# Kernel tuning notes

Measured on AMD Instinct MI355X. Metric: run time of the kernel, lower is better.

## Reference

```python
import jax, jax.numpy as jnp
import numpy as np

B, D, A, M = 262144, 128, 32, 100


def setup_inputs() -> dict:
    key = jax.random.key(0)
    ks = jax.random.split(key, 8)
    s = 0.05
    return {
        "state": jax.random.normal(ks[0], (B, D), jnp.float32),
        "action": jax.random.normal(ks[1], (B, A), jnp.float32),
        "next_state": jax.random.normal(ks[2], (B, D), jnp.float32),
        "seen": jax.random.normal(ks[3], (M, D), jnp.float32),
        "W1": jax.random.normal(ks[4], (D, D + A), jnp.float32) * s,
        "b1": jnp.zeros((D,), jnp.float32),
        "W2": jax.random.normal(ks[5], (D, D), jnp.float32) * s,
        "b2": jnp.zeros((D,), jnp.float32),
        "Wf": jax.random.normal(ks[6], (D, D), jnp.float32) * s,
        "bf": jnp.zeros((D,), jnp.float32),
    }


def reference(state, action, next_state, seen, W1, b1, W2, b2, Wf, bf):
    # predictor: Linear(D+A -> D) -> ReLU -> Linear(D -> D)   (torch: y = x W^T + b)
    x = jnp.concatenate([state, action], axis=-1)            # [B, D+A]
    h = jax.nn.relu(x @ W1.T + b1)                           # [B, D]
    predicted_next = h @ W2.T + b2                           # [B, D]

    # feature_extractor: Linear(D -> D) -> ReLU
    feat = lambda z: jax.nn.relu(z @ Wf.T + bf)
    features_actual = feat(next_state)                       # [B, D]
    features_pred = feat(predicted_next)                     # [B, D]

    # per-sample MSE prediction error (features_actual detached in original)
    fa_sg = jax.lax.stop_gradient(features_actual)
    pred_error = jnp.mean((features_pred - fa_sg) ** 2, axis=-1)  # [B]

    # 1-NN L2 distance to memory buffer, batched via the ||a-b||^2 expansion
    # (avoids materializing [B, M, D])
    a2 = jnp.sum(features_actual ** 2, axis=-1, keepdims=True)    # [B, 1]
    s2 = jnp.sum(seen ** 2, axis=-1)                              # [M]
    d2 = a2 + s2[None, :] - 2.0 * (features_actual @ seen.T)      # [B, M]
    min_dist = jnp.sqrt(jnp.maximum(jnp.min(d2, axis=-1), 0.0))   # [B]
    novelty = jnp.minimum(1.0, min_dist / 10.0)                   # [B]

    curiosity_reward = pred_error * 0.5 + novelty * 0.5
    return jnp.stack([pred_error, novelty, curiosity_reward])     # [3, B]
```

## Files before the change

### kernel.cpp

```cpp
#include <hip/hip_runtime.h>
#include <hip/hip_bf16.h>
#include <math.h>

#define B_TOT 262144

typedef __attribute__((ext_vector_type(8))) short v8s;
typedef __attribute__((ext_vector_type(4))) float v4f;

#define WS_W1 0
#define WS_W2 20480
#define WS_WF 36864
#define WS_SEEN 53248
#define WS_S2_BYTES 135168

__device__ __forceinline__ unsigned short f2bf(float f) {
  union { float f; unsigned u; } cv; cv.f = f;
  unsigned u = cv.u;
  return (unsigned short)((u + 0x7FFFu + ((u >> 16) & 1u)) >> 16);
}
__device__ __forceinline__ float bf2f(unsigned short h) {
  union { unsigned u; float f; } cv; cv.u = ((unsigned)h) << 16;
  return cv.f;
}
__device__ __forceinline__ unsigned f2bf2(float x, float y) {
  float2 f; f.x = x; f.y = y;
  __hip_bfloat162 h = __float22bfloat162_rn(f);
  union { __hip_bfloat162 h; unsigned u; } cv; cv.h = h;
  return cv.u;
}

__global__ void curiosity_prep(const float* __restrict__ W1, const float* __restrict__ W2,
                               const float* __restrict__ Wf, const float* __restrict__ seen,
                               unsigned short* __restrict__ wsb, float* __restrict__ s2) {
  int bid = blockIdx.x;
  if (bid < 264) {
    int idx = bid * 256 + (int)threadIdx.x;
    if (idx < 20480) {
      int f = idx >> 9, r = idx & 511, L = r >> 3, j = r & 7;
      int t = f / 5, c = f - t * 5;
      int n = t * 16 + (L & 15), k = c * 32 + (L >> 4) * 8 + j;
      wsb[idx] = f2bf(W1[n * 160 + k]);
    } else if (idx < 36864) {
      int e = idx - 20480;
      int f = e >> 9, r = e & 511, L = r >> 3, j = r & 7;
      int t = f >> 2, c = f & 3;
      int n = t * 16 + (L & 15), k = c * 32 + (L >> 4) * 8 + j;
      wsb[idx] = f2bf(W2[n * 128 + k]);
    } else if (idx < 53248) {
      int e = idx - 36864;
      int f = e >> 9, r = e & 511, L = r >> 3, j = r & 7;
      int t = f >> 2, c = f & 3;
      int n = t * 16 + (L & 15), k = c * 32 + (L >> 4) * 8 + j;
      wsb[idx] = f2bf(Wf[n * 128 + k]);
    } else {
      int e = idx - 53248;
      int f = e >> 9, r = e & 511, L = r >> 3, j = r & 7;
      int t = f >> 2, c = f & 3;
      int n = t * 16 + (L & 15), k = c * 32 + (L >> 4) * 8 + j;
      float v = (n < 100) ? seen[n * 128 + k] : 0.f;
      wsb[idx] = f2bf(v);
    }
  } else {
    int wv = (int)threadIdx.x >> 6, lane = (int)threadIdx.x & 63;
    int mm = (bid - 264) * 4 + wv;
    float s;
    if (mm < 100) {
      float v0 = seen[mm * 128 + lane], v1 = seen[mm * 128 + 64 + lane];
      s = v0 * v0 + v1 * v1;
#pragma unroll
      for (int msk = 1; msk < 64; msk <<= 1) s += __shfl_xor(s, msk, 64);
    } else {
      s = 1e30f;
    }
    if (lane == 0) s2[mm] = s;
  }
}

__device__ __forceinline__ void stage16x128(const float* __restrict__ src,
                                            unsigned short* buf, int lane) {
  float4 v[8];
#pragma unroll
  for (int i = 0; i < 8; ++i) {
    int flat = i * 64 + lane;
    v[i] = *(const float4*)(src + (flat >> 5) * 128 + (flat & 31) * 4);
  }
#pragma unroll
  for (int i = 0; i < 8; ++i) {
    int flat = i * 64 + lane;
    uint2 p;
    p.x = f2bf2(v[i].x, v[i].y);
    p.y = f2bf2(v[i].z, v[i].w);
    *(uint2*)(buf + (flat >> 5) * 136 + (flat & 31) * 4) = p;
  }
}
__device__ __forceinline__ void stage16x32(const float* __restrict__ src,
                                           unsigned short* buf, int lane) {
  float4 v[2];
#pragma unroll
  for (int i = 0; i < 2; ++i) {
    int flat = i * 64 + lane;
    v[i] = *(const float4*)(src + (flat >> 3) * 32 + (flat & 7) * 4);
  }
#pragma unroll
  for (int i = 0; i < 2; ++i) {
    int flat = i * 64 + lane;
    uint2 p;
    p.x = f2bf2(v[i].x, v[i].y);
    p.y = f2bf2(v[i].z, v[i].w);
    *(uint2*)(buf + (flat >> 3) * 136 + (flat & 7) * 4) = p;
  }
}
__device__ __forceinline__ v8s read_frag(const unsigned short* buf, int m, int q, int c) {
  return *(const v8s*)(buf + m * 136 + c * 32 + q * 8);
}
__device__ __forceinline__ v8s wfrag(const unsigned short* __restrict__ wsb,
                                     int base, int fragIdx, int lane) {
  return *(const v8s*)(wsb + base + fragIdx * 512 + lane * 8);
}

__global__ __launch_bounds__(256, 3) void curiosity_main(
    const float* __restrict__ state, const float* __restrict__ action,
    const float* __restrict__ next_state,
    const float* __restrict__ b1, const float* __restrict__ b2,
    const float* __restrict__ bfv,
    const unsigned short* __restrict__ wsb, const float* __restrict__ s2g,
    float* __restrict__ out) {
  __shared__ __attribute__((aligned(16))) unsigned short s_int[4][2][2176];
  __shared__ float s_o[3][128];

  const int tid = (int)threadIdx.x;
  const int w = tid >> 6, lane = tid & 63;
  const int m = lane & 15, q = lane >> 4;
  const int rowblk = (int)blockIdx.x * 128 + w * 32;

  unsigned short* buf[2] = { &s_int[w][0][0], &s_int[w][1][0] };

  float bv1[8];
#pragma unroll
  for (int tg = 0; tg < 8; ++tg) bv1[tg] = b1[tg * 16 + m];

  v8s a1[2][5];
  stage16x32(action + (size_t)(rowblk) * 32, buf[0], lane);
  stage16x32(action + (size_t)(rowblk + 16) * 32, buf[1], lane);
  a1[0][4] = *(const v8s*)(buf[0] + m * 136 + q * 8);
  a1[1][4] = *(const v8s*)(buf[1] + m * 136 + q * 8);
  stage16x128(state + (size_t)(rowblk) * 128, buf[0], lane);
  stage16x128(state + (size_t)(rowblk + 16) * 128, buf[1], lane);
#pragma unroll
  for (int c = 0; c < 4; ++c) {
    a1[0][c] = read_frag(buf[0], m, q, c);
    a1[1][c] = read_frag(buf[1], m, q, c);
  }

  float bv2[8];
#pragma unroll
  for (int tg = 0; tg < 8; ++tg) bv2[tg] = b2[tg * 16 + m];

#pragma unroll
  for (int hf = 0; hf < 2; ++hf) {
    v8s bfr[20];
#pragma unroll
    for (int c = 0; c < 5; ++c)
#pragma unroll
      for (int tl = 0; tl < 4; ++tl)
        bfr[c * 4 + tl] = wfrag(wsb, WS_W1, (hf * 4 + tl) * 5 + c, lane);
    v4f acc[2][4] = {};
#pragma unroll
    for (int c = 0; c < 5; ++c)
#pragma unroll
      for (int tl = 0; tl < 4; ++tl) {
        acc[0][tl] = __builtin_amdgcn_mfma_f32_16x16x32_bf16(a1[0][c], bfr[c * 4 + tl], acc[0][tl], 0, 0, 0);
        acc[1][tl] = __builtin_amdgcn_mfma_f32_16x16x32_bf16(a1[1][c], bfr[c * 4 + tl], acc[1][tl], 0, 0, 0);
      }
#pragma unroll
    for (int tl = 0; tl < 4; ++tl) {
      int tg = hf * 4 + tl;
      float bv = bv1[tg];
#pragma unroll
      for (int tt = 0; tt < 2; ++tt)
#pragma unroll
        for (int r = 0; r < 4; r += 2) {
          unsigned p = f2bf2(fmaxf(acc[tt][tl][r] + bv, 0.f),
                             fmaxf(acc[tt][tl][r + 1] + bv, 0.f));
          buf[tt][(q * 4 + r) * 136 + tg * 16 + m] = (unsigned short)p;
          buf[tt][(q * 4 + r + 1) * 136 + tg * 16 + m] = (unsigned short)(p >> 16);
        }
    }
  }

  v8s af[2][4];
#pragma unroll
  for (int c = 0; c < 4; ++c) {
    af[0][c] = read_frag(buf[0], m, q, c);
    af[1][c] = read_frag(buf[1], m, q, c);
  }
  float bvf[8];
#pragma unroll
  for (int tg = 0; tg < 8; ++tg) bvf[tg] = bfv[tg * 16 + m];

#pragma unroll
  for (int hf = 0; hf < 2; ++hf) {
    v8s bfr[16];
#pragma unroll
    for (int c = 0; c < 4; ++c)
#pragma unroll
      for (int tl = 0; tl < 4; ++tl)
        bfr[c * 4 + tl] = wfrag(wsb, WS_W2, (hf * 4 + tl) * 4 + c, lane);
    v4f acc[2][4] = {};
#pragma unroll
    for (int c = 0; c < 4; ++c)
#pragma unroll
      for (int tl = 0; tl < 4; ++tl) {
        acc[0][tl] = __builtin_amdgcn_mfma_f32_16x16x32_bf16(af[0][c], bfr[c * 4 + tl], acc[0][tl], 0, 0, 0);
        acc[1][tl] = __builtin_amdgcn_mfma_f32_16x16x32_bf16(af[1][c], bfr[c * 4 + tl], acc[1][tl], 0, 0, 0);
      }
#pragma unroll
    for (int tl = 0; tl < 4; ++tl) {
      int tg = hf * 4 + tl;
      float bv = bv2[tg];
#pragma unroll
      for (int tt = 0; tt < 2; ++tt)
#pragma unroll
        for (int r = 0; r < 4; r += 2) {
          unsigned p = f2bf2(acc[tt][tl][r] + bv, acc[tt][tl][r + 1] + bv);
          buf[tt][(q * 4 + r) * 136 + tg * 16 + m] = (unsigned short)p;
          buf[tt][(q * 4 + r + 1) * 136 + tg * 16 + m] = (unsigned short)(p >> 16);
        }
    }
  }

  v8s a4[2][4], a3[2][4];
#pragma unroll
  for (int c = 0; c < 4; ++c) {
    a4[0][c] = read_frag(buf[0], m, q, c);
    a4[1][c] = read_frag(buf[1], m, q, c);
  }
  stage16x128(next_state + (size_t)(rowblk) * 128, buf[0], lane);
  stage16x128(next_state + (size_t)(rowblk + 16) * 128, buf[1], lane);
#pragma unroll
  for (int c = 0; c < 4; ++c) {
    a3[0][c] = read_frag(buf[0], m, q, c);
    a3[1][c] = read_frag(buf[1], m, q, c);
  }

  float s2v[7];
#pragma unroll
  for (int tl = 0; tl < 7; ++tl) s2v[tl] = s2g[tl * 16 + m];

  unsigned fa_pk[2][16];
  float a2s[2][4] = {};
#pragma unroll
  for (int hf = 0; hf < 2; ++hf) {
    v8s bfr[16];
#pragma unroll
    for (int c = 0; c < 4; ++c)
#pragma unroll
      for (int tl = 0; tl < 4; ++tl)
        bfr[c * 4 + tl] = wfrag(wsb, WS_WF, (hf * 4 + tl) * 4 + c, lane);
    v4f acc[2][4] = {};
#pragma unroll
    for (int c = 0; c < 4; ++c)
#pragma unroll
      for (int tl = 0; tl < 4; ++tl) {
        acc[0][tl] = __builtin_amdgcn_mfma_f32_16x16x32_bf16(a3[0][c], bfr[c * 4 + tl], acc[0][tl], 0, 0, 0);
        acc[1][tl] = __builtin_amdgcn_mfma_f32_16x16x32_bf16(a3[1][c], bfr[c * 4 + tl], acc[1][tl], 0, 0, 0);
      }
#pragma unroll
    for (int tl = 0; tl < 4; ++tl) {
      int tg = hf * 4 + tl;
      float bv = bvf[tg];
#pragma unroll
      for (int tt = 0; tt < 2; ++tt)
#pragma unroll
        for (int rp = 0; rp < 2; ++rp) {
          int r = rp * 2;
          unsigned p = f2bf2(fmaxf(acc[tt][tl][r] + bv, 0.f),
                             fmaxf(acc[tt][tl][r + 1] + bv, 0.f));
          fa_pk[hf][tl * 4 + tt * 2 + rp] = p;
          buf[tt][(q * 4 + r) * 136 + tg * 16 + m] = (unsigned short)p;
          buf[tt][(q * 4 + r + 1) * 136 + tg * 16 + m] = (unsigned short)(p >> 16);
          float flo = bf2f((unsigned short)p), fhi = bf2f((unsigned short)(p >> 16));
          a2s[tt][r] += flo * flo;
          a2s[tt][r + 1] += fhi * fhi;
        }
    }
  }

  float pe[2][4] = {};
#pragma unroll
  for (int hf = 0; hf < 2; ++hf) {
    v8s bfr[16];
#pragma unroll
    for (int c = 0; c < 4; ++c)
#pragma unroll
      for (int tl = 0; tl < 4; ++tl)
        bfr[c * 4 + tl] = wfrag(wsb, WS_WF, (hf * 4 + tl) * 4 + c, lane);
    v4f acc[2][4] = {};
#pragma unroll
    for (int c = 0; c < 4; ++c)
#pragma unroll
      for (int tl = 0; tl < 4; ++tl) {
        acc[0][tl] = __builtin_amdgcn_mfma_f32_16x16x32_bf16(a4[0][c], bfr[c * 4 + tl], acc[0][tl], 0, 0, 0);
        acc[1][tl] = __builtin_amdgcn_mfma_f32_16x16x32_bf16(a4[1][c], bfr[c * 4 + tl], acc[1][tl], 0, 0, 0);
      }
#pragma unroll
    for (int tl = 0; tl < 4; ++tl) {
      int tg = hf * 4 + tl;
      float bv = bvf[tg];
#pragma unroll
      for (int tt = 0; tt < 2; ++tt)
#pragma unroll
        for (int rp = 0; rp < 2; ++rp) {
          int r = rp * 2;
          unsigned p = fa_pk[hf][tl * 4 + tt * 2 + rp];
          float d0 = fmaxf(acc[tt][tl][r] + bv, 0.f) - bf2f((unsigned short)p);
          float d1 = fmaxf(acc[tt][tl][r + 1] + bv, 0.f) - bf2f((unsigned short)(p >> 16));
          pe[tt][r] += d0 * d0;
          pe[tt][r + 1] += d1 * d1;
        }
    }
  }

#pragma unroll
  for (int tt = 0; tt < 2; ++tt)
#pragma unroll
    for (int r = 0; r < 4; ++r)
#pragma unroll
      for (int msk = 1; msk < 16; msk <<= 1) {
        pe[tt][r] += __shfl_xor(pe[tt][r], msk, 16);
        a2s[tt][r] += __shfl_xor(a2s[tt][r], msk, 16);
      }

  v8s a5[2][4];
#pragma unroll
  for (int c = 0; c < 4; ++c) {
    a5[0][c] = read_frag(buf[0], m, q, c);
    a5[1][c] = read_frag(buf[1], m, q, c);
  }
  float dmin[2][4] = {{3.4e38f, 3.4e38f, 3.4e38f, 3.4e38f},
                      {3.4e38f, 3.4e38f, 3.4e38f, 3.4e38f}};
  {
    v8s bfr[16];
#pragma unroll
    for (int tl = 0; tl < 4; ++tl)
#pragma unroll
      for (int c = 0; c < 4; ++c)
        bfr[tl * 4 + c] = wfrag(wsb, WS_SEEN, tl * 4 + c, lane);
#pragma unroll
    for (int tl = 0; tl < 4; ++tl) {
      v4f g0 = {}, g1 = {};
#pragma unroll
      for (int c = 0; c < 4; ++c) {
        g0 = __builtin_amdgcn_mfma_f32_16x16x32_bf16(a5[0][c], bfr[tl * 4 + c], g0, 0, 0, 0);
        g1 = __builtin_amdgcn_mfma_f32_16x16x32_bf16(a5[1][c], bfr[tl * 4 + c], g1, 0, 0, 0);
      }
      float s2x = s2v[tl];
#pragma unroll
      for (int r = 0; r < 4; ++r) {
        dmin[0][r] = fminf(dmin[0][r], a2s[0][r] + s2x - 2.f * g0[r]);
        dmin[1][r] = fminf(dmin[1][r], a2s[1][r] + s2x - 2.f * g1[r]);
      }
    }
  }
  {
    v8s bfr[12];
#pragma unroll
    for (int tl = 0; tl < 3; ++tl)
#pragma unroll
      for (int c = 0; c < 4; ++c)
        bfr[tl * 4 + c] = wfrag(wsb, WS_SEEN, (tl + 4) * 4 + c, lane);
#pragma unroll
    for (int tl = 0; tl < 3; ++tl) {
      v4f g0 = {}, g1 = {};
#pragma unroll
      for (int c = 0; c < 4; ++c) {
        g0 = __builtin_amdgcn_mfma_f32_16x16x32_bf16(a5[0][c], bfr[tl * 4 + c], g0, 0, 0, 0);
        g1 = __builtin_amdgcn_mfma_f32_16x16x32_bf16(a5[1][c], bfr[tl * 4 + c], g1, 0, 0, 0);
      }
      float s2x = s2v[tl + 4];
#pragma unroll
      for (int r = 0; r < 4; ++r) {
        dmin[0][r] = fminf(dmin[0][r], a2s[0][r] + s2x - 2.f * g0[r]);
        dmin[1][r] = fminf(dmin[1][r], a2s[1][r] + s2x - 2.f * g1[r]);
      }
    }
  }
#pragma unroll
  for (int tt = 0; tt < 2; ++tt)
#pragma unroll
    for (int r = 0; r < 4; ++r)
#pragma unroll
      for (int msk = 1; msk < 16; msk <<= 1)
        dmin[tt][r] = fminf(dmin[tt][r], __shfl_xor(dmin[tt][r], msk, 16));

  if (m == 0) {
#pragma unroll
    for (int tt = 0; tt < 2; ++tt)
#pragma unroll
      for (int r = 0; r < 4; ++r) {
        int rl = w * 32 + tt * 16 + q * 4 + r;
        float p = pe[tt][r] * (1.f / 128.f);
        float nov = fminf(1.f, sqrtf(fmaxf(dmin[tt][r], 0.f)) * 0.1f);
        s_o[0][rl] = p;
        s_o[1][rl] = nov;
        s_o[2][rl] = 0.5f * (p + nov);
      }
  }
  __syncthreads();
  const size_t base = (size_t)blockIdx.x * 128;
  for (int idx = tid; idx < 384; idx += 256) {
    int j = idx >> 7, r = idx & 127;
    out[(size_t)j * B_TOT + base + r] = s_o[j][r];
  }
}

extern "C" void kernel_launch(void* const* d_in, const int* in_sizes, int n_in,
                              void* d_out, int out_size, void* d_ws, size_t ws_size,
                              hipStream_t stream) {
  const float* state      = (const float*)d_in[0];
  const float* action     = (const float*)d_in[1];
  const float* next_state = (const float*)d_in[2];
  const float* seen       = (const float*)d_in[3];
  const float* W1         = (const float*)d_in[4];
  const float* b1         = (const float*)d_in[5];
  const float* W2         = (const float*)d_in[6];
  const float* b2         = (const float*)d_in[7];
  const float* Wf         = (const float*)d_in[8];
  const float* bf_        = (const float*)d_in[9];

  unsigned short* wsb = (unsigned short*)d_ws;
  float* s2 = (float*)((char*)d_ws + WS_S2_BYTES);

  curiosity_prep<<<292, 256, 0, stream>>>(W1, W2, Wf, seen, wsb, s2);
  curiosity_main<<<2048, 256, 0, stream>>>(state, action, next_state, b1, b2, bf_,
                                           wsb, s2, (float*)d_out);
}
```

Before: 375.7 us.

## Load inputs directly into MFMA fragments, prefetch next_state, fuse feature GEMMs

Result: no change. 371.8 us (-1.0%).

```diff
diff --git a/kernel.cpp b/kernel.cpp
--- a/kernel.cpp
+++ b/kernel.cpp
@@ -76,40 +76,15 @@
   }
 }
 
-__device__ __forceinline__ void stage16x128(const float* __restrict__ src,
-                                            unsigned short* buf, int lane) {
-  float4 v[8];
-#pragma unroll
-  for (int i = 0; i < 8; ++i) {
-    int flat = i * 64 + lane;
-    v[i] = *(const float4*)(src + (flat >> 5) * 128 + (flat & 31) * 4);
-  }
-#pragma unroll
-  for (int i = 0; i < 8; ++i) {
-    int flat = i * 64 + lane;
-    uint2 p;
-    p.x = f2bf2(v[i].x, v[i].y);
-    p.y = f2bf2(v[i].z, v[i].w);
-    *(uint2*)(buf + (flat >> 5) * 136 + (flat & 31) * 4) = p;
-  }
-}
-__device__ __forceinline__ void stage16x32(const float* __restrict__ src,
-                                           unsigned short* buf, int lane) {
-  float4 v[2];
-#pragma unroll
-  for (int i = 0; i < 2; ++i) {
-    int flat = i * 64 + lane;
-    v[i] = *(const float4*)(src + (flat >> 3) * 32 + (flat & 7) * 4);
-  }
-#pragma unroll
-  for (int i = 0; i < 2; ++i) {
-    int flat = i * 64 + lane;
-    uint2 p;
-    p.x = f2bf2(v[i].x, v[i].y);
-    p.y = f2bf2(v[i].z, v[i].w);
-    *(uint2*)(buf + (flat >> 3) * 136 + (flat & 7) * 4) = p;
-  }
-}
+__device__ __forceinline__ v8s cvt_frag(float4 lo, float4 hi) {
+  union { v8s v; unsigned u[4]; } r;
+  r.u[0] = f2bf2(lo.x, lo.y);
+  r.u[1] = f2bf2(lo.z, lo.w);
+  r.u[2] = f2bf2(hi.x, hi.y);
+  r.u[3] = f2bf2(hi.z, hi.w);
+  return r.v;
+}
+
 __device__ __forceinline__ v8s read_frag(const unsigned short* buf, int m, int q, int c) {
   return *(const v8s*)(buf + m * 136 + c * 32 + q * 8);
 }
@@ -135,26 +110,40 @@
 
   unsigned short* buf[2] = { &s_int[w][0][0], &s_int[w][1][0] };
 
-  float bv1[8];
+  const float* st0 = state + (size_t)(rowblk + m) * 128 + q * 8;
+  const float* st1 = st0 + 16 * 128;
+  const float* ac0 = action + (size_t)(rowblk + m) * 32 + q * 8;
+  const float* ac1 = ac0 + 16 * 32;
+  const float* np0 = next_state + (size_t)(rowblk + m) * 128 + q * 8;
+  const float* np1 = np0 + 16 * 128;
+
+  float4 sv[2][4][2], av[2][2];
+#pragma unroll
+  for (int c = 0; c < 4; ++c) {
+    sv[0][c][0] = *(const float4*)(st0 + c * 32);
+    sv[0][c][1] = *(const float4*)(st0 + c * 32 + 4);
+    sv[1][c][0] = *(const float4*)(st1 + c * 32);
+    sv[1][c][1] = *(const float4*)(st1 + c * 32 + 4);
+  }
+  av[0][0] = *(const float4*)(ac0); av[0][1] = *(const float4*)(ac0 + 4);
+  av[1][0] = *(const float4*)(ac1); av[1][1] = *(const float4*)(ac1 + 4);
+
+  float bv1[8], bv2[8], bvf[8];
 #pragma unroll
   for (int tg = 0; tg < 8; ++tg) bv1[tg] = b1[tg * 16 + m];
+#pragma unroll
+  for (int tg = 0; tg < 8; ++tg) bv2[tg] = b2[tg * 16 + m];
+#pragma unroll
+  for (int tg = 0; tg < 8; ++tg) bvf[tg] = bfv[tg * 16 + m];
 
   v8s a1[2][5];
-  stage16x32(action + (size_t)(rowblk) * 32, buf[0], lane);
-  stage16x32(action + (size_t)(rowblk + 16) * 32, buf[1], lane);
-  a1[0][4] = *(const v8s*)(buf[0] + m * 136 + q * 8);
-  a1[1][4] = *(const v8s*)(buf[1] + m * 136 + q * 8);
-  stage16x128(state + (size_t)(rowblk) * 128, buf[0], lane);
-  stage16x128(state + (size_t)(rowblk + 16) * 128, buf[1], lane);
-#pragma unroll
-  for (int c = 0; c < 4; ++c) {
-    a1[0][c] = read_frag(buf[0], m, q, c);
-    a1[1][c] = read_frag(buf[1], m, q, c);
-  }
-
-  float bv2[8];
-#pragma unroll
-  for (int tg = 0; tg < 8; ++tg) bv2[tg] = b2[tg * 16 + m];
+#pragma unroll
+  for (int c = 0; c < 4; ++c) {
+    a1[0][c] = cvt_frag(sv[0][c][0], sv[0][c][1]);
+    a1[1][c] = cvt_frag(sv[1][c][0], sv[1][c][1]);
+  }
+  a1[0][4] = cvt_frag(av[0][0], av[0][1]);
+  a1[1][4] = cvt_frag(av[1][0], av[1][1]);
 
 #pragma unroll
   for (int hf = 0; hf < 2; ++hf) {
@@ -188,18 +177,31 @@
     }
   }
 
+  float4 n0v[4][2], n1v[4][2];
+#pragma unroll
+  for (int c = 0; c < 4; ++c) {
+    n0v[c][0] = *(const float4*)(np0 + c * 32);
+    n0v[c][1] = *(const float4*)(np0 + c * 32 + 4);
+  }
+
   v8s af[2][4];
 #pragma unroll
   for (int c = 0; c < 4; ++c) {
     af[0][c] = read_frag(buf[0], m, q, c);
     af[1][c] = read_frag(buf[1], m, q, c);
   }
-  float bvf[8];
-#pragma unroll
-  for (int tg = 0; tg < 8; ++tg) bvf[tg] = bfv[tg * 16 + m];
-
+  v8s a3[2][4];
 #pragma unroll
   for (int hf = 0; hf < 2; ++hf) {
+    if (hf == 1) {
+#pragma unroll
+      for (int c = 0; c < 4; ++c) a3[0][c] = cvt_frag(n0v[c][0], n0v[c][1]);
+#pragma unroll
+      for (int c = 0; c < 4; ++c) {
+        n1v[c][0] = *(const float4*)(np1 + c * 32);
+        n1v[c][1] = *(const float4*)(np1 + c * 32 + 4);
+      }
+    }
     v8s bfr[16];
 #pragma unroll
     for (int c = 0; c < 4; ++c)
@@ -229,95 +231,59 @@
     }
   }
 
-  v8s a4[2][4], a3[2][4];
+  v8s a4[2][4];
 #pragma unroll
   for (int c = 0; c < 4; ++c) {
     a4[0][c] = read_frag(buf[0], m, q, c);
     a4[1][c] = read_frag(buf[1], m, q, c);
   }
-  stage16x128(next_state + (size_t)(rowblk) * 128, buf[0], lane);
-  stage16x128(next_state + (size_t)(rowblk + 16) * 128, buf[1], lane);
-#pragma unroll
-  for (int c = 0; c < 4; ++c) {
-    a3[0][c] = read_frag(buf[0], m, q, c);
-    a3[1][c] = read_frag(buf[1], m, q, c);
-  }
+#pragma unroll
+  for (int c = 0; c < 4; ++c) a3[1][c] = cvt_frag(n1v[c][0], n1v[c][1]);
 
   float s2v[7];
 #pragma unroll
   for (int tl = 0; tl < 7; ++tl) s2v[tl] = s2g[tl * 16 + m];
 
-  unsigned fa_pk[2][16];
+  float pe[2][4] = {};
   float a2s[2][4] = {};
 #pragma unroll
   for (int hf = 0; hf < 2; ++hf) {
-    v8s bfr[16];
-#pragma unroll
-    for (int c = 0; c < 4; ++c)
-#pragma unroll
-      for (int tl = 0; tl < 4; ++tl)
-        bfr[c * 4 + tl] = wfrag(wsb, WS_WF, (hf * 4 + tl) * 4 + c, lane);
-    v4f acc[2][4] = {};
-#pragma unroll
-    for (int c = 0; c < 4; ++c)
-#pragma unroll
-      for (int tl = 0; tl < 4; ++tl) {
-        acc[0][tl] = __builtin_amdgcn_mfma_f32_16x16x32_bf16(a3[0][c], bfr[c * 4 + tl], acc[0][tl], 0, 0, 0);
-        acc[1][tl] = __builtin_amdgcn_mfma_f32_16x16x32_bf16(a3[1][c], bfr[c * 4 + tl], acc[1][tl], 0, 0, 0);
-      }
 #pragma unroll
     for (int tl = 0; tl < 4; ++tl) {
+      v8s bfr[4];
+#pragma unroll
+      for (int c = 0; c < 4; ++c)
+        bfr[c] = wfrag(wsb, WS_WF, (hf * 4 + tl) * 4 + c, lane);
+      v4f fa0 = {}, fa1 = {}, fp0 = {}, fp1 = {};
+#pragma unroll
+      for (int c = 0; c < 4; ++c) {
+        fa0 = __builtin_amdgcn_mfma_f32_16x16x32_bf16(a3[0][c], bfr[c], fa0, 0, 0, 0);
+        fa1 = __builtin_amdgcn_mfma_f32_16x16x32_bf16(a3[1][c], bfr[c], fa1, 0, 0, 0);
+        fp0 = __builtin_amdgcn_mfma_f32_16x16x32_bf16(a4[0][c], bfr[c], fp0, 0, 0, 0);
+        fp1 = __builtin_amdgcn_mfma_f32_16x16x32_bf16(a4[1][c], bfr[c], fp1, 0, 0, 0);
+      }
       int tg = hf * 4 + tl;
       float bv = bvf[tg];
 #pragma unroll
-      for (int tt = 0; tt < 2; ++tt)
+      for (int tt = 0; tt < 2; ++tt) {
+        const v4f& fav = tt ? fa1 : fa0;
+        const v4f& fpv = tt ? fp1 : fp0;
 #pragma unroll
         for (int rp = 0; rp < 2; ++rp) {
           int r = rp * 2;
-          unsigned p = f2bf2(fmaxf(acc[tt][tl][r] + bv, 0.f),
-                             fmaxf(acc[tt][tl][r + 1] + bv, 0.f));
-          fa_pk[hf][tl * 4 + tt * 2 + rp] = p;
+          unsigned p = f2bf2(fmaxf(fav[r] + bv, 0.f),
+                             fmaxf(fav[r + 1] + bv, 0.f));
           buf[tt][(q * 4 + r) * 136 + tg * 16 + m] = (unsigned short)p;
           buf[tt][(q * 4 + r + 1) * 136 + tg * 16 + m] = (unsigned short)(p >> 16);
           float flo = bf2f((unsigned short)p), fhi = bf2f((unsigned short)(p >> 16));
           a2s[tt][r] += flo * flo;
           a2s[tt][r + 1] += fhi * fhi;
-        }
-    }
-  }
-
-  float pe[2][4] = {};
-#pragma unroll
-  for (int hf = 0; hf < 2; ++hf) {
-    v8s bfr[16];
-#pragma unroll
-    for (int c = 0; c < 4; ++c)
-#pragma unroll
-      for (int tl = 0; tl < 4; ++tl)
-        bfr[c * 4 + tl] = wfrag(wsb, WS_WF, (hf * 4 + tl) * 4 + c, lane);
-    v4f acc[2][4] = {};
-#pragma unroll
-    for (int c = 0; c < 4; ++c)
-#pragma unroll
-      for (int tl = 0; tl < 4; ++tl) {
-        acc[0][tl] = __builtin_amdgcn_mfma_f32_16x16x32_bf16(a4[0][c], bfr[c * 4 + tl], acc[0][tl], 0, 0, 0);
-        acc[1][tl] = __builtin_amdgcn_mfma_f32_16x16x32_bf16(a4[1][c], bfr[c * 4 + tl], acc[1][tl], 0, 0, 0);
-      }
-#pragma unroll
-    for (int tl = 0; tl < 4; ++tl) {
-      int tg = hf * 4 + tl;
-      float bv = bvf[tg];
-#pragma unroll
-      for (int tt = 0; tt < 2; ++tt)
-#pragma unroll
-        for (int rp = 0; rp < 2; ++rp) {
-          int r = rp * 2;
-          unsigned p = fa_pk[hf][tl * 4 + tt * 2 + rp];
-          float d0 = fmaxf(acc[tt][tl][r] + bv, 0.f) - bf2f((unsigned short)p);
-          float d1 = fmaxf(acc[tt][tl][r + 1] + bv, 0.f) - bf2f((unsigned short)(p >> 16));
+          float d0 = fmaxf(fpv[r] + bv, 0.f) - flo;
+          float d1 = fmaxf(fpv[r + 1] + bv, 0.f) - fhi;
           pe[tt][r] += d0 * d0;
           pe[tt][r + 1] += d1 * d1;
         }
+      }
     }
   }
 
```
